# Optimization experiments

Hardware: AMD Instinct MI355X
Metric: run time of the kernel (lower is better)

Reference implementation:

```python
import jax, jax.numpy as jnp
import numpy as np

COST_CLASS = 1.0
COST_MASK = 5.0
COST_DICE = 5.0


def _sample_points(masks, coords):
    """Bilinear grid_sample (align_corners=False, zero padding).

    masks:  [N, H, W] float
    coords: [P, 2] in [0, 1], (x, y) order as in torch grid_sample
    returns [N, P]
    """
    H, W = masks.shape[-2], masks.shape[-1]
    # torch: grid = 2*c - 1; pixel = ((grid+1)*size - 1)/2 = c*size - 0.5
    x = coords[:, 0] * W - 0.5
    y = coords[:, 1] * H - 0.5
    x0 = jnp.floor(x)
    y0 = jnp.floor(y)
    tx = (x - x0).astype(masks.dtype)
    ty = (y - y0).astype(masks.dtype)
    x0i = x0.astype(jnp.int32)
    y0i = y0.astype(jnp.int32)

    def gather(ix, iy):
        valid = ((ix >= 0) & (ix < W) & (iy >= 0) & (iy < H)).astype(masks.dtype)
        v = masks[:, jnp.clip(iy, 0, H - 1), jnp.clip(ix, 0, W - 1)]  # [N, P]
        return v * valid

    v00 = gather(x0i, y0i)
    v01 = gather(x0i + 1, y0i)
    v10 = gather(x0i, y0i + 1)
    v11 = gather(x0i + 1, y0i + 1)
    return (v00 * (1 - tx) * (1 - ty) + v01 * tx * (1 - ty)
            + v10 * (1 - tx) * ty + v11 * tx * ty)


def _cost_one(pred_mask, pred_logits, tgt_mask, labels, coords):
    # pred_mask [Q,H,W], pred_logits [Q,C], tgt_mask [T,H,W], labels [T], coords [P,2]
    probs = jax.nn.softmax(pred_logits, axis=-1)          # [Q, C]
    cost_class = -probs[:, labels]                        # [Q, T]

    pm = _sample_points(pred_mask, coords)                # [Q, P] logits
    tm = _sample_points(tgt_mask, coords)                 # [T, P] in [0,1]
    P = pm.shape[1]

    # pair-wise sigmoid BCE: BCE(x, 1) = softplus(-x), BCE(x, 0) = softplus(x)
    ce_pos = jax.nn.softplus(-pm) / P                     # [Q, P]
    ce_neg = jax.nn.softplus(pm) / P                      # [Q, P]
    cost_mask = ce_pos @ tm.T + ce_neg @ (1.0 - tm).T     # [Q, T]

    # pair-wise dice
    sig = jax.nn.sigmoid(pm)                              # [Q, P]
    numerator = 2.0 * (sig @ tm.T)                        # [Q, T]
    denominator = sig.sum(-1)[:, None] + tm.sum(-1)[None, :]
    cost_dice = 1.0 - (numerator + 1.0) / (denominator + 1.0)

    return COST_MASK * cost_mask + COST_CLASS * cost_class + COST_DICE * cost_dice


def setup_inputs() -> dict:
    key = jax.random.key(0)
    k1, k2, k3, k4, k5 = jax.random.split(key, 5)
    B, Q, C, T, H, W, P = 8, 150, 134, 32, 160, 160, 12544
    masks_queries_logits = jax.random.normal(k1, (B, Q, H, W), dtype=jnp.float32)
    class_queries_logits = jax.random.normal(k2, (B, Q, C), dtype=jnp.float32)
    # binary target masks
    mask_labels = (jax.random.uniform(k3, (B, T, H, W)) > 0.5).astype(jnp.float32)
    class_labels = jax.random.randint(k4, (B, T), 0, 133, dtype=jnp.int64)
    point_coords = jax.random.uniform(k5, (B, P, 2), dtype=jnp.float32)
    return {
        "masks_queries_logits": masks_queries_logits,
        "class_queries_logits": class_queries_logits,
        "mask_labels": mask_labels,
        "class_labels": class_labels,
        "point_coords": point_coords,
    }


def reference(masks_queries_logits, class_queries_logits, mask_labels, class_labels, point_coords):
    # Returns the per-sample cost matrices [B, Q, T] (the GPU-side work of the
    # matcher). The scipy Hungarian assignment on these matrices is CPU-bound
    # and intentionally excluded from the kernel baseline.
    cost = jax.vmap(_cost_one)(
        masks_queries_logits, class_queries_logits, mask_labels, class_labels, point_coords
    )
    return cost
```

## Files before the change

### kernel.cpp

```cpp
#include <hip/hip_runtime.h>
#include <hip/hip_bf16.h>
#include <hip/hip_fp16.h>
#include <math.h>

#define B_ 8
#define Q_ 150
#define QP_ 160
#define C_ 134
#define T_ 32
#define H_ 160
#define W_ 160
#define P_ 12544
#define HW_ (H_ * W_)
#define HW4_ (HW_ / 4)

#define SBLK 1024
#define SBATCH 3
#define STAIL 256
#define SEG_ 56
#define KSEG 224
#define KITER 7
#define DSTRIDE (2 * B_ * QP_ * T_)

typedef __attribute__((ext_vector_type(8))) short short8;
typedef __attribute__((ext_vector_type(4))) float floatx4;

struct Samp {
  int i00, i01, i10, i11;
  float w00, w01, w10, w11;
};

__device__ __forceinline__ Samp make_samp(float cx, float cy) {
  float x = cx * (float)W_ - 0.5f;
  float y = cy * (float)H_ - 0.5f;
  float x0f = floorf(x), y0f = floorf(y);
  float tx = x - x0f, ty = y - y0f;
  int x0 = (int)x0f, y0 = (int)y0f;
  int x1 = x0 + 1, y1 = y0 + 1;
  bool vx0 = (x0 >= 0) && (x0 < W_);
  bool vx1 = (x1 >= 0) && (x1 < W_);
  bool vy0 = (y0 >= 0) && (y0 < H_);
  bool vy1 = (y1 >= 0) && (y1 < H_);
  int cx0 = min(max(x0, 0), W_ - 1), cx1 = min(max(x1, 0), W_ - 1);
  int cy0 = min(max(y0, 0), H_ - 1), cy1 = min(max(y1, 0), H_ - 1);
  Samp s;
  s.i00 = cy0 * W_ + cx0;
  s.i01 = cy0 * W_ + cx1;
  s.i10 = cy1 * W_ + cx0;
  s.i11 = cy1 * W_ + cx1;
  float w00 = (1.f - tx) * (1.f - ty);
  float w01 = tx * (1.f - ty);
  float w10 = (1.f - tx) * ty;
  float w11 = tx * ty;
  s.w00 = (vx0 && vy0) ? w00 : 0.f;
  s.w01 = (vx1 && vy0) ? w01 : 0.f;
  s.w10 = (vx0 && vy1) ? w10 : 0.f;
  s.w11 = (vx1 && vy1) ? w11 : 0.f;
  return s;
}

__device__ __forceinline__ float waveSum(float v) {
#pragma unroll
  for (int m = 32; m >= 1; m >>= 1) v += __shfl_xor(v, m, 64);
  return v;
}
__device__ __forceinline__ float waveMax(float v) {
#pragma unroll
  for (int m = 32; m >= 1; m >>= 1) v = fmaxf(v, __shfl_xor(v, m, 64));
  return v;
}

__device__ __forceinline__ unsigned short f2bf(float x) {
  union { __hip_bfloat16 h; unsigned short u; } cv;
  cv.h = __float2bfloat16(x);
  return cv.u;
}
__device__ __forceinline__ float bf2f(unsigned short u) {
  return __uint_as_float(((unsigned int)u) << 16);
}
__device__ __forceinline__ float h2f(unsigned short u) {
  union { __half h; unsigned short u; } cv;
  cv.u = u;
  return __half2float(cv.h);
}
__device__ __forceinline__ unsigned short f2h(float x) {
  union { __half h; unsigned short u; } cv;
  cv.h = __float2half(x);
  return cv.u;
}

__launch_bounds__(256) __global__
void samp_kernel(const float* __restrict__ coords,
                 unsigned int* __restrict__ sIdx,
                 uint2* __restrict__ sW) {
  int i = blockIdx.x * 256 + threadIdx.x;
  float2 cc = ((const float2*)coords)[i];
  Samp s = make_samp(cc.x, cc.y);
  int dx = s.i01 - s.i00;
  int dy = (s.i10 != s.i00) ? 1 : 0;
  sIdx[i] = (unsigned)s.i00 | ((unsigned)dx << 15) | ((unsigned)dy << 16);
  uint2 w;
  w.x = (unsigned)f2h(s.w00) | ((unsigned)f2h(s.w01) << 16);
  w.y = (unsigned)f2h(s.w10) | ((unsigned)f2h(s.w11) << 16);
  sW[i] = w;
}

__device__ __forceinline__ float lds_sample(const unsigned short* img,
                                            unsigned iv, uint2 wv) {
  int i00 = iv & 0x7fff;
  int i01 = i00 + ((iv >> 15) & 1);
  int ir = (iv & 0x10000) ? W_ : 0;
  return h2f(wv.x & 0xffff) * bf2f(img[i00]) +
         h2f(wv.x >> 16) * bf2f(img[i01]) +
         h2f(wv.y & 0xffff) * bf2f(img[i00 + ir]) +
         h2f(wv.y >> 16) * bf2f(img[i01 + ir]);
}

__launch_bounds__(SBLK, 8) __global__
void sample_kernel(const float* __restrict__ masks_q,
                   const float* __restrict__ mask_labels,
                   const unsigned int* __restrict__ sIdx,
                   const uint2* __restrict__ sW,
                   unsigned short* __restrict__ pmh,
                   unsigned short* __restrict__ tmh,
                   float* __restrict__ S_sp, float* __restrict__ S_sig,
                   float* __restrict__ S_tm) {
  __shared__ unsigned short img[HW_];
  __shared__ float red[32];
  const int x = blockIdx.x;
  const int b = blockIdx.y;
  const int tid = threadIdx.x;
  const bool isPm = (x < Q_);

  const float* src = isPm ? (masks_q + ((size_t)b * Q_ + x) * HW_)
                          : (mask_labels + ((size_t)b * T_ + (x - Q_)) * HW_);
  const float4* s4 = (const float4*)src;
#pragma unroll
  for (int c = 0; c < 6; ++c) {
    int i = c * SBLK + tid;
    float4 v = s4[i];
    ushort4 u;
    u.x = f2bf(v.x); u.y = f2bf(v.y); u.z = f2bf(v.z); u.w = f2bf(v.w);
    *(ushort4*)&img[4 * i] = u;
  }
  if (tid < HW4_ - 6 * SBLK) {
    int i = 6 * SBLK + tid;
    float4 v = s4[i];
    ushort4 u;
    u.x = f2bf(v.x); u.y = f2bf(v.y); u.z = f2bf(v.z); u.w = f2bf(v.w);
    *(ushort4*)&img[4 * i] = u;
  }
  __syncthreads();

  const unsigned int* sIdxB = sIdx + (size_t)b * P_;
  const uint2* sWB = sW + (size_t)b * P_;

  if (isPm) {
    unsigned short* dst = pmh + ((size_t)b * QP_ + x) * P_;
    float ssp = 0.f, ssg = 0.f;
    for (int c = 0; c < SBATCH; ++c) {
      int p = c * (4 * SBLK) + tid;
      unsigned iv[4];
      uint2 wv[4];
      float v[4];
#pragma unroll
      for (int j = 0; j < 4; ++j) {
        iv[j] = sIdxB[p + j * SBLK];
        wv[j] = sWB[p + j * SBLK];
      }
#pragma unroll
      for (int j = 0; j < 4; ++j) v[j] = lds_sample(img, iv[j], wv[j]);
#pragma unroll
      for (int j = 0; j < 4; ++j) {
        float pm = v[j];
        float e = __expf(-fabsf(pm));
        float r = __builtin_amdgcn_rcpf(1.f + e);
        float sp = fmaxf(pm, 0.f) - __logf(r);
        float sg = (pm >= 0.f) ? r : e * r;
        ssp += sp;
        ssg += sg;
        dst[p + j * SBLK] = f2bf(pm);
      }
    }
    if (tid < STAIL) {
      int p = SBATCH * 4 * SBLK + tid;
      float pm = lds_sample(img, sIdxB[p], sWB[p]);
      float e = __expf(-fabsf(pm));
      float r = __builtin_amdgcn_rcpf(1.f + e);
      float sp = fmaxf(pm, 0.f) - __logf(r);
      float sg = (pm >= 0.f) ? r : e * r;
      ssp += sp;
      ssg += sg;
      dst[p] = f2bf(pm);
    }
    ssp = waveSum(ssp);
    ssg = waveSum(ssg);
    int w = tid >> 6;
    if ((tid & 63) == 0) {
      red[w] = ssp;
      red[16 + w] = ssg;
    }
    __syncthreads();
    if (tid == 0) {
      float a = 0.f, bb = 0.f;
#pragma unroll
      for (int i = 0; i < 16; ++i) { a += red[i]; bb += red[16 + i]; }
      S_sp[b * Q_ + x] = a;
      S_sig[b * Q_ + x] = bb;
    }
  } else {
    const int t = x - Q_;
    unsigned short* dst = tmh + ((size_t)b * T_ + t) * P_;
    float stm = 0.f;
    for (int c = 0; c < SBATCH; ++c) {
      int p = c * (4 * SBLK) + tid;
      unsigned iv[4];
      uint2 wv[4];
#pragma unroll
      for (int j = 0; j < 4; ++j) {
        iv[j] = sIdxB[p + j * SBLK];
        wv[j] = sWB[p + j * SBLK];
      }
#pragma unroll
      for (int j = 0; j < 4; ++j) {
        float v = lds_sample(img, iv[j], wv[j]);
        stm += v;
        dst[p + j * SBLK] = f2bf(v);
      }
    }
    if (tid < STAIL) {
      int p = SBATCH * 4 * SBLK + tid;
      float v = lds_sample(img, sIdxB[p], sWB[p]);
      stm += v;
      dst[p] = f2bf(v);
    }
    stm = waveSum(stm);
    int w = tid >> 6;
    if ((tid & 63) == 0) red[w] = stm;
    __syncthreads();
    if (tid == 0) {
      float a = 0.f;
#pragma unroll
      for (int i = 0; i < 16; ++i) a += red[i];
      S_tm[b * T_ + t] = a;
    }
  }
}

__device__ __forceinline__ short8 sig_frag(short8 a) {
  short8 out;
#pragma unroll
  for (int j = 0; j < 8; ++j) {
    float x = bf2f((unsigned short)a[j]);
    float e = __expf(-fabsf(x));
    float r = __builtin_amdgcn_rcpf(1.f + e);
    float sg = (x >= 0.f) ? r : e * r;
    out[j] = (short)f2bf(sg);
  }
  return out;
}

__launch_bounds__(320) __global__
void gemm_kernel(const unsigned short* __restrict__ pmh,
                 const unsigned short* __restrict__ tmh,
                 float* __restrict__ accP) {
  const int b = blockIdx.y;
  const int seg = blockIdx.x;
  const int w = threadIdx.x >> 6;
  const int l = threadIdx.x & 63;
  const int quad = l >> 4;
  const int mrow = l & 15;

  const unsigned short* pmb = pmh + ((size_t)b * QP_ + w * 32) * P_;
  const unsigned short* tmb = tmh + (size_t)b * T_ * P_;

  floatx4 aL[2][2];
  floatx4 aS[2][2];
#pragma unroll
  for (int i = 0; i < 2; ++i)
#pragma unroll
    for (int j = 0; j < 2; ++j) {
      aL[i][j] = (floatx4){0.f, 0.f, 0.f, 0.f};
      aS[i][j] = (floatx4){0.f, 0.f, 0.f, 0.f};
    }

  const int kbase = seg * KSEG;
#pragma unroll
  for (int ki = 0; ki < KITER; ++ki) {
    const int k0 = kbase + ki * 32 + quad * 8;
    short8 a0 = *(const short8*)(pmb + (size_t)(0 * 16 + mrow) * P_ + k0);
    short8 a1 = *(const short8*)(pmb + (size_t)(1 * 16 + mrow) * P_ + k0);
    short8 b0 = *(const short8*)(tmb + (size_t)(0 * 16 + mrow) * P_ + k0);
    short8 b1 = *(const short8*)(tmb + (size_t)(1 * 16 + mrow) * P_ + k0);
    short8 s0 = sig_frag(a0);
    short8 s1 = sig_frag(a1);
    aL[0][0] = __builtin_amdgcn_mfma_f32_16x16x32_bf16(a0, b0, aL[0][0], 0, 0, 0);
    aL[0][1] = __builtin_amdgcn_mfma_f32_16x16x32_bf16(a0, b1, aL[0][1], 0, 0, 0);
    aL[1][0] = __builtin_amdgcn_mfma_f32_16x16x32_bf16(a1, b0, aL[1][0], 0, 0, 0);
    aL[1][1] = __builtin_amdgcn_mfma_f32_16x16x32_bf16(a1, b1, aL[1][1], 0, 0, 0);
    aS[0][0] = __builtin_amdgcn_mfma_f32_16x16x32_bf16(s0, b0, aS[0][0], 0, 0, 0);
    aS[0][1] = __builtin_amdgcn_mfma_f32_16x16x32_bf16(s0, b1, aS[0][1], 0, 0, 0);
    aS[1][0] = __builtin_amdgcn_mfma_f32_16x16x32_bf16(s1, b0, aS[1][0], 0, 0, 0);
    aS[1][1] = __builtin_amdgcn_mfma_f32_16x16x32_bf16(s1, b1, aS[1][1], 0, 0, 0);
  }

  float* base = accP + (size_t)seg * DSTRIDE;
#pragma unroll
  for (int mtl = 0; mtl < 2; ++mtl)
#pragma unroll
    for (int nt = 0; nt < 2; ++nt)
#pragma unroll
      for (int r = 0; r < 4; ++r) {
        int q = w * 32 + mtl * 16 + quad * 4 + r;
        int t = nt * 16 + mrow;
        base[((size_t)(0 * B_ + b) * QP_ + q) * T_ + t] = aL[mtl][nt][r];
        base[((size_t)(1 * B_ + b) * QP_ + q) * T_ + t] = aS[mtl][nt][r];
      }
}

__launch_bounds__(256) __global__
void reduce_kernel(const float* __restrict__ accP, float* __restrict__ accD) {
  int i = blockIdx.x * 256 + threadIdx.x;
  float s = 0.f;
#pragma unroll
  for (int seg = 0; seg < SEG_; ++seg) s += accP[(size_t)seg * DSTRIDE + i];
  accD[i] = s;
}

__launch_bounds__(64) __global__
void final_kernel(const float* __restrict__ class_q,
                  const int* __restrict__ labels,
                  const float* __restrict__ accD,
                  const float* __restrict__ S_sp,
                  const float* __restrict__ S_sig,
                  const float* __restrict__ S_tm,
                  float* __restrict__ out) {
  const int bq = blockIdx.x;
  const int b = bq / Q_;
  const int q = bq % Q_;
  const int l = threadIdx.x;
  const float* cl = class_q + (size_t)bq * C_;

  float v = -INFINITY;
  for (int c = l; c < C_; c += 64) v = fmaxf(v, cl[c]);
  float m = waveMax(v);
  float e = 0.f;
  for (int c = l; c < C_; c += 64) e += __expf(cl[c] - m);
  float den = waveSum(e);

  if (l < T_) {
    int t = l;
    int lbl = labels[b * T_ + t];
    float prob = __expf(cl[lbl] - m) / den;
    float Dlin = accD[((size_t)(0 * B_ + b) * QP_ + q) * T_ + t];
    float Dsig = accD[((size_t)(1 * B_ + b) * QP_ + q) * T_ + t];
    float cmask = (S_sp[bq] - Dlin) * (1.f / (float)P_);
    float dice = 1.f - (2.f * Dsig + 1.f) / (S_sig[bq] + S_tm[b * T_ + t] + 1.f);
    out[(size_t)bq * T_ + t] = 5.f * cmask + 5.f * dice - prob;
  }
}

extern "C" void kernel_launch(void* const* d_in, const int* in_sizes, int n_in,
                              void* d_out, int out_size, void* d_ws,
                              size_t ws_size, hipStream_t stream) {
  const float* masks_q = (const float*)d_in[0];
  const float* class_q = (const float*)d_in[1];
  const float* mask_labels = (const float*)d_in[2];
  const int* class_labels = (const int*)d_in[3];
  const float* coords = (const float*)d_in[4];
  float* out = (float*)d_out;

  float* accD = (float*)d_ws;
  float* accP = accD + DSTRIDE;
  uint2* sW = (uint2*)(accP + (size_t)SEG_ * DSTRIDE);
  unsigned int* sIdx = (unsigned int*)(sW + (size_t)B_ * P_);
  float* S_sp = (float*)(sIdx + (size_t)B_ * P_);
  float* S_sig = S_sp + B_ * Q_;
  float* S_tm = S_sig + B_ * Q_;
  unsigned short* pmh = (unsigned short*)(S_tm + B_ * T_);
  unsigned short* tmh = pmh + (size_t)B_ * QP_ * P_;

  samp_kernel<<<(B_ * P_) / 256, 256, 0, stream>>>(coords, sIdx, sW);
  sample_kernel<<<dim3(Q_ + T_, B_), SBLK, 0, stream>>>(
      masks_q, mask_labels, sIdx, sW, pmh, tmh, S_sp, S_sig, S_tm);
  gemm_kernel<<<dim3(SEG_, B_), 320, 0, stream>>>(pmh, tmh, accP);
  reduce_kernel<<<DSTRIDE / 256, 256, 0, stream>>>(accP, accD);
  final_kernel<<<B_ * Q_, 64, 0, stream>>>(class_q, class_labels, accD, S_sp,
                                           S_sig, S_tm, out);
}
```

Measured before the change: 240.7 us.

## Store sampled images as fp16 even/odd pair layout and use dot2 bilinear

The LDS image copy moves from bf16 to fp16 and is stored twice: an even-aligned copy and an odd-shifted copy. Each horizontal pixel pair can then be read as one aligned 32-bit load and combined with fp16 dot2 instructions, which cuts the bilinear sample from four scalar LDS reads to two. Edge cases where x1==x0 are folded into the weights at setup. The intermediate pm/tm buffers and the GEMM switch to fp16 MFMA to match. LDS use doubles, so occupancy per CU drops (launch bounds change from 8 to 4), and fp16 has less range than bf16 for large logits.

```diff
diff --git a/kernel.cpp b/kernel.cpp
--- a/kernel.cpp
+++ b/kernel.cpp
@@ -22,7 +22,11 @@
 #define KITER 7
 #define DSTRIDE (2 * B_ * QP_ * T_)
 
-typedef __attribute__((ext_vector_type(8))) short short8;
+#define LDS_BYTES (2 * HW_ * 2 + 128)
+#define ODD_BASE (2 * HW_)
+
+typedef __attribute__((ext_vector_type(8))) _Float16 half8;
+typedef __attribute__((ext_vector_type(2))) _Float16 half2v;
 typedef __attribute__((ext_vector_type(4))) float floatx4;
 
 struct Samp {
@@ -70,14 +74,6 @@
   return v;
 }
 
-__device__ __forceinline__ unsigned short f2bf(float x) {
-  union { __hip_bfloat16 h; unsigned short u; } cv;
-  cv.h = __float2bfloat16(x);
-  return cv.u;
-}
-__device__ __forceinline__ float bf2f(unsigned short u) {
-  return __uint_as_float(((unsigned int)u) << 16);
-}
 __device__ __forceinline__ float h2f(unsigned short u) {
   union { __half h; unsigned short u; } cv;
   cv.u = u;
@@ -87,6 +83,17 @@
   union { __half h; unsigned short u; } cv;
   cv.h = __float2half(x);
   return cv.u;
+}
+
+__device__ __forceinline__ float dot2h(unsigned int pv, unsigned int wv,
+                                       float acc) {
+#if __has_builtin(__builtin_amdgcn_fdot2)
+  return __builtin_amdgcn_fdot2(__builtin_bit_cast(half2v, pv),
+                                __builtin_bit_cast(half2v, wv), acc, false);
+#else
+  return acc + h2f(pv & 0xffff) * h2f(wv & 0xffff) +
+         h2f(pv >> 16) * h2f(wv >> 16);
+#endif
 }
 
 __launch_bounds__(256) __global__
@@ -96,27 +103,31 @@
   int i = blockIdx.x * 256 + threadIdx.x;
   float2 cc = ((const float2*)coords)[i];
   Samp s = make_samp(cc.x, cc.y);
-  int dx = s.i01 - s.i00;
+  bool dx = (s.i01 != s.i00);
   int dy = (s.i10 != s.i00) ? 1 : 0;
-  sIdx[i] = (unsigned)s.i00 | ((unsigned)dx << 15) | ((unsigned)dy << 16);
+  float w00e = dx ? s.w00 : (s.w00 + s.w01);
+  float w01e = dx ? s.w01 : 0.f;
+  float w10e = dx ? s.w10 : (s.w10 + s.w11);
+  float w11e = dx ? s.w11 : 0.f;
+  sIdx[i] = (unsigned)s.i00 | ((unsigned)dy << 16);
   uint2 w;
-  w.x = (unsigned)f2h(s.w00) | ((unsigned)f2h(s.w01) << 16);
-  w.y = (unsigned)f2h(s.w10) | ((unsigned)f2h(s.w11) << 16);
+  w.x = (unsigned)f2h(w00e) | ((unsigned)f2h(w01e) << 16);
+  w.y = (unsigned)f2h(w10e) | ((unsigned)f2h(w11e) << 16);
   sW[i] = w;
 }
 
-__device__ __forceinline__ float lds_sample(const unsigned short* img,
-                                            unsigned iv, uint2 wv) {
-  int i00 = iv & 0x7fff;
-  int i01 = i00 + ((iv >> 15) & 1);
-  int ir = (iv & 0x10000) ? W_ : 0;
-  return h2f(wv.x & 0xffff) * bf2f(img[i00]) +
-         h2f(wv.x >> 16) * bf2f(img[i01]) +
-         h2f(wv.y & 0xffff) * bf2f(img[i00 + ir]) +
-         h2f(wv.y >> 16) * bf2f(img[i01 + ir]);
-}
-
-__launch_bounds__(SBLK, 8) __global__
+__device__ __forceinline__ float lds_sample(const char* lds, unsigned iv,
+                                            uint2 wv) {
+  int i00 = iv & 0xffff & 0x7fff;
+  int odd = i00 & 1;
+  int off = 2 * i00 + (odd ? (ODD_BASE - 2) : 0);
+  int ir2 = (iv & 0x10000) ? (2 * W_) : 0;
+  unsigned pair0 = *(const unsigned*)(lds + off);
+  unsigned pair1 = *(const unsigned*)(lds + off + ir2);
+  return dot2h(pair0, wv.x, dot2h(pair1, wv.y, 0.f));
+}
+
+__launch_bounds__(SBLK, 4) __global__
 void sample_kernel(const float* __restrict__ masks_q,
                    const float* __restrict__ mask_labels,
                    const unsigned int* __restrict__ sIdx,
@@ -125,8 +136,11 @@
                    unsigned short* __restrict__ tmh,
                    float* __restrict__ S_sp, float* __restrict__ S_sig,
                    float* __restrict__ S_tm) {
-  __shared__ unsigned short img[HW_];
-  __shared__ float red[32];
+  extern __shared__ char lds[];
+  unsigned short* imgE = (unsigned short*)lds;
+  unsigned short* imgO = (unsigned short*)(lds + ODD_BASE);
+  float* red = (float*)(lds + 2 * ODD_BASE);
+
   const int x = blockIdx.x;
   const int b = blockIdx.y;
   const int tid = threadIdx.x;
@@ -135,20 +149,19 @@
   const float* src = isPm ? (masks_q + ((size_t)b * Q_ + x) * HW_)
                           : (mask_labels + ((size_t)b * T_ + (x - Q_)) * HW_);
   const float4* s4 = (const float4*)src;
-#pragma unroll
-  for (int c = 0; c < 6; ++c) {
+
+#pragma unroll
+  for (int c = 0; c < 7; ++c) {
     int i = c * SBLK + tid;
-    float4 v = s4[i];
-    ushort4 u;
-    u.x = f2bf(v.x); u.y = f2bf(v.y); u.z = f2bf(v.z); u.w = f2bf(v.w);
-    *(ushort4*)&img[4 * i] = u;
-  }
-  if (tid < HW4_ - 6 * SBLK) {
-    int i = 6 * SBLK + tid;
-    float4 v = s4[i];
-    ushort4 u;
-    u.x = f2bf(v.x); u.y = f2bf(v.y); u.z = f2bf(v.z); u.w = f2bf(v.w);
-    *(ushort4*)&img[4 * i] = u;
+    if (c < 6 || tid < HW4_ - 6 * SBLK) {
+      float4 v = s4[i];
+      float nxt = (i < HW4_ - 1) ? src[4 * i + 4] : 0.f;
+      ushort4 e, o;
+      e.x = f2h(v.x); e.y = f2h(v.y); e.z = f2h(v.z); e.w = f2h(v.w);
+      o.x = e.y; o.y = e.z; o.z = e.w; o.w = f2h(nxt);
+      *(ushort4*)&imgE[4 * i] = e;
+      *(ushort4*)&imgO[4 * i] = o;
+    }
   }
   __syncthreads();
 
@@ -169,7 +182,7 @@
         wv[j] = sWB[p + j * SBLK];
       }
 #pragma unroll
-      for (int j = 0; j < 4; ++j) v[j] = lds_sample(img, iv[j], wv[j]);
+      for (int j = 0; j < 4; ++j) v[j] = lds_sample(lds, iv[j], wv[j]);
 #pragma unroll
       for (int j = 0; j < 4; ++j) {
         float pm = v[j];
@@ -179,19 +192,19 @@
         float sg = (pm >= 0.f) ? r : e * r;
         ssp += sp;
         ssg += sg;
-        dst[p + j * SBLK] = f2bf(pm);
+        dst[p + j * SBLK] = f2h(pm);
       }
     }
     if (tid < STAIL) {
       int p = SBATCH * 4 * SBLK + tid;
-      float pm = lds_sample(img, sIdxB[p], sWB[p]);
+      float pm = lds_sample(lds, sIdxB[p], sWB[p]);
       float e = __expf(-fabsf(pm));
       float r = __builtin_amdgcn_rcpf(1.f + e);
       float sp = fmaxf(pm, 0.f) - __logf(r);
       float sg = (pm >= 0.f) ? r : e * r;
       ssp += sp;
       ssg += sg;
-      dst[p] = f2bf(pm);
+      dst[p] = f2h(pm);
     }
     ssp = waveSum(ssp);
     ssg = waveSum(ssg);
@@ -223,16 +236,16 @@
       }
 #pragma unroll
       for (int j = 0; j < 4; ++j) {
-        float v = lds_sample(img, iv[j], wv[j]);
+        float v = lds_sample(lds, iv[j], wv[j]);
         stm += v;
-        dst[p + j * SBLK] = f2bf(v);
+        dst[p + j * SBLK] = f2h(v);
       }
     }
     if (tid < STAIL) {
       int p = SBATCH * 4 * SBLK + tid;
-      float v = lds_sample(img, sIdxB[p], sWB[p]);
+      float v = lds_sample(lds, sIdxB[p], sWB[p]);
       stm += v;
-      dst[p] = f2bf(v);
+      dst[p] = f2h(v);
     }
     stm = waveSum(stm);
     int w = tid >> 6;
@@ -247,15 +260,15 @@
   }
 }
 
-__device__ __forceinline__ short8 sig_frag(short8 a) {
-  short8 out;
+__device__ __forceinline__ half8 sig_frag(half8 a) {
+  half8 out;
 #pragma unroll
   for (int j = 0; j < 8; ++j) {
-    float x = bf2f((unsigned short)a[j]);
+    float x = (float)a[j];
     float e = __expf(-fabsf(x));
     float r = __builtin_amdgcn_rcpf(1.f + e);
     float sg = (x >= 0.f) ? r : e * r;
-    out[j] = (short)f2bf(sg);
+    out[j] = (_Float16)sg;
   }
   return out;
 }
@@ -288,20 +301,20 @@
 #pragma unroll
   for (int ki = 0; ki < KITER; ++ki) {
     const int k0 = kbase + ki * 32 + quad * 8;
-    short8 a0 = *(const short8*)(pmb + (size_t)(0 * 16 + mrow) * P_ + k0);
-    short8 a1 = *(const short8*)(pmb + (size_t)(1 * 16 + mrow) * P_ + k0);
-    short8 b0 = *(const short8*)(tmb + (size_t)(0 * 16 + mrow) * P_ + k0);
-    short8 b1 = *(const short8*)(tmb + (size_t)(1 * 16 + mrow) * P_ + k0);
-    short8 s0 = sig_frag(a0);
-    short8 s1 = sig_frag(a1);
-    aL[0][0] = __builtin_amdgcn_mfma_f32_16x16x32_bf16(a0, b0, aL[0][0], 0, 0, 0);
-    aL[0][1] = __builtin_amdgcn_mfma_f32_16x16x32_bf16(a0, b1, aL[0][1], 0, 0, 0);
-    aL[1][0] = __builtin_amdgcn_mfma_f32_16x16x32_bf16(a1, b0, aL[1][0], 0, 0, 0);
-    aL[1][1] = __builtin_amdgcn_mfma_f32_16x16x32_bf16(a1, b1, aL[1][1], 0, 0, 0);
-    aS[0][0] = __builtin_amdgcn_mfma_f32_16x16x32_bf16(s0, b0, aS[0][0], 0, 0, 0);
-    aS[0][1] = __builtin_amdgcn_mfma_f32_16x16x32_bf16(s0, b1, aS[0][1], 0, 0, 0);
-    aS[1][0] = __builtin_amdgcn_mfma_f32_16x16x32_bf16(s1, b0, aS[1][0], 0, 0, 0);
-    aS[1][1] = __builtin_amdgcn_mfma_f32_16x16x32_bf16(s1, b1, aS[1][1], 0, 0, 0);
+    half8 a0 = *(const half8*)(pmb + (size_t)(0 * 16 + mrow) * P_ + k0);
+    half8 a1 = *(const half8*)(pmb + (size_t)(1 * 16 + mrow) * P_ + k0);
+    half8 b0 = *(const half8*)(tmb + (size_t)(0 * 16 + mrow) * P_ + k0);
+    half8 b1 = *(const half8*)(tmb + (size_t)(1 * 16 + mrow) * P_ + k0);
+    half8 s0 = sig_frag(a0);
+    half8 s1 = sig_frag(a1);
+    aL[0][0] = __builtin_amdgcn_mfma_f32_16x16x32_f16(a0, b0, aL[0][0], 0, 0, 0);
+    aL[0][1] = __builtin_amdgcn_mfma_f32_16x16x32_f16(a0, b1, aL[0][1], 0, 0, 0);
+    aL[1][0] = __builtin_amdgcn_mfma_f32_16x16x32_f16(a1, b0, aL[1][0], 0, 0, 0);
+    aL[1][1] = __builtin_amdgcn_mfma_f32_16x16x32_f16(a1, b1, aL[1][1], 0, 0, 0);
+    aS[0][0] = __builtin_amdgcn_mfma_f32_16x16x32_f16(s0, b0, aS[0][0], 0, 0, 0);
+    aS[0][1] = __builtin_amdgcn_mfma_f32_16x16x32_f16(s0, b1, aS[0][1], 0, 0, 0);
+    aS[1][0] = __builtin_amdgcn_mfma_f32_16x16x32_f16(s1, b0, aS[1][0], 0, 0, 0);
+    aS[1][1] = __builtin_amdgcn_mfma_f32_16x16x32_f16(s1, b1, aS[1][1], 0, 0, 0);
   }
 
   float* base = accP + (size_t)seg * DSTRIDE;
@@ -380,8 +393,13 @@
   unsigned short* pmh = (unsigned short*)(S_tm + B_ * T_);
   unsigned short* tmh = pmh + (size_t)B_ * QP_ * P_;
 
+  static int lds_configured = 0;
+  (void)lds_configured;
+  hipFuncSetAttribute((const void*)sample_kernel,
+                      hipFuncAttributeMaxDynamicSharedMemorySize, LDS_BYTES);
+
   samp_kernel<<<(B_ * P_) / 256, 256, 0, stream>>>(coords, sIdx, sW);
-  sample_kernel<<<dim3(Q_ + T_, B_), SBLK, 0, stream>>>(
+  sample_kernel<<<dim3(Q_ + T_, B_), SBLK, LDS_BYTES, stream>>>(
       masks_q, mask_labels, sIdx, sW, pmh, tmh, S_sp, S_sig, S_tm);
   gemm_kernel<<<dim3(SEG_, B_), 320, 0, stream>>>(pmh, tmh, accP);
   reduce_kernel<<<DSTRIDE / 256, 256, 0, stream>>>(accP, accD);
```

Result: slower. 250.0 us (+3.9%).
